# Kernel tuning notes

Measured on AMD Instinct MI355X. Metric: run time of the kernel, lower is better.

The kernel has to match this reference:

```python
import jax, jax.numpy as jnp
import numpy as np

B, S, H, D = 4, 2048, 16, 128

def setup_inputs() -> dict:
    key = jax.random.key(0)
    kq, kk, kv = jax.random.split(key, 3)
    shape = (B, S, H, D)
    return {
        "q": jax.random.normal(kq, shape, dtype=jnp.float32),
        "k": jax.random.normal(kk, shape, dtype=jnp.float32),
        "v": jax.random.normal(kv, shape, dtype=jnp.float32),
    }

def reference(q, k, v):
    # Fused recurrent linear attention (causal, unnormalized):
    #   H_t = H_{t-1} + k_t v_t^T ;  o_t = (scale * q_t) @ H_t
    scale = jnp.asarray(q.shape[-1], q.dtype) ** -0.5
    # move seq axis to front for scan: [S, B, H, D]
    qs = jnp.moveaxis(q, 1, 0) * scale
    ks = jnp.moveaxis(k, 1, 0)
    vs = jnp.moveaxis(v, 1, 0)

    def step(h, qkv):
        qt, kt, vt = qkv  # each [B, H, D]
        h = h + kt[..., :, None] * vt[..., None, :]  # [B, H, Dk, Dv]
        o = jnp.einsum('bhk,bhkv->bhv', qt, h)       # [B, H, Dv]
        return h, o

    h0 = jnp.zeros((q.shape[0], q.shape[2], q.shape[3], v.shape[3]), dtype=q.dtype)
    _, o = jax.lax.scan(step, h0, (qs, ks, vs))
    return jnp.moveaxis(o, 0, 1)  # [B, S, H, D]
```

## Files before the change

kernel.cpp:

```cpp
#include <hip/hip_runtime.h>


#define Bc 4
#define Sq 2048
#define Hh 16
#define Dd 128
#define RS (Hh * Dd)
#define Cc 128
#define NCH (Sq / Cc)
#define BHt (Bc * Hh)

using frag_ab = __attribute__((ext_vector_type(8))) short;
using frag_cd = __attribute__((ext_vector_type(4))) float;

__device__ __forceinline__ unsigned short f2bf(float f) {
  union { float f; unsigned u; } x; x.f = f;
  unsigned r = x.u + 0x7FFFu + ((x.u >> 16) & 1u);
  return (unsigned short)(r >> 16);
}
__device__ __forceinline__ float bf2f(unsigned short h) {
  union { unsigned u; float f; } x; x.u = ((unsigned)h) << 16; return x.f;
}
__device__ __forceinline__ int sw64(int r, int c) {
  return r * 64 + ((((c >> 3) ^ (r & 7)) << 3) | (c & 7));
}
__device__ __forceinline__ int sw128(int r, int c) {
  return r * 128 + ((((c >> 3) ^ (r & 15)) << 3) | (c & 7));
}

#define SCALE 0.08838834764831845f

__global__ __launch_bounds__(256) void ph1_ktv(const float* __restrict__ kg,
                                               const float* __restrict__ vg,
                                               unsigned short* __restrict__ st) {
  __shared__ unsigned short KT[128 * 64];
  __shared__ unsigned short VT[128 * 64];
  const int tid = threadIdx.x;
  const int bid = blockIdx.x;
  const int bh = bid >> 4, n = bid & 15;
  const int b = bh >> 4, h = bh & 15;
  const size_t cbase = (size_t)b * Sq * RS + (size_t)n * Cc * RS + (size_t)h * Dd;
  const int w = tid >> 6, L = tid & 63;
  const int wr = w >> 1, wc = w & 1, li = L & 15, q4 = L >> 4;

  frag_cd acc[4][4];
#pragma unroll
  for (int i = 0; i < 4; ++i)
#pragma unroll
    for (int j = 0; j < 4; ++j) acc[i][j] = (frag_cd){0.f, 0.f, 0.f, 0.f};

  for (int half = 0; half < 2; ++half) {
    __syncthreads();
#pragma unroll
    for (int it = 0; it < 8; ++it) {
      const int sl = (tid & 15) | ((it & 3) << 4);
      const int c0 = ((tid >> 4) | ((it >> 2) << 4)) << 2;
      const int t = 64 * half + sl;
      const float4 k4 = *(const float4*)(kg + cbase + (size_t)t * RS + c0);
      const float4 v4 = *(const float4*)(vg + cbase + (size_t)t * RS + c0);
      KT[sw64(c0 + 0, sl)] = f2bf(k4.x);
      KT[sw64(c0 + 1, sl)] = f2bf(k4.y);
      KT[sw64(c0 + 2, sl)] = f2bf(k4.z);
      KT[sw64(c0 + 3, sl)] = f2bf(k4.w);
      VT[sw64(c0 + 0, sl)] = f2bf(v4.x);
      VT[sw64(c0 + 1, sl)] = f2bf(v4.y);
      VT[sw64(c0 + 2, sl)] = f2bf(v4.z);
      VT[sw64(c0 + 3, sl)] = f2bf(v4.w);
    }
    __syncthreads();
#pragma unroll
    for (int kt = 0; kt < 2; ++kt) {
      frag_ab af[4], bf_[4];
#pragma unroll
      for (int mt = 0; mt < 4; ++mt)
        af[mt] = *(const frag_ab*)&VT[sw64(64 * wr + 16 * mt + li, 32 * kt + 8 * q4)];
#pragma unroll
      for (int nt = 0; nt < 4; ++nt)
        bf_[nt] = *(const frag_ab*)&KT[sw64(64 * wc + 16 * nt + li, 32 * kt + 8 * q4)];
#pragma unroll
      for (int mt = 0; mt < 4; ++mt)
#pragma unroll
        for (int nt = 0; nt < 4; ++nt)
          acc[mt][nt] = __builtin_amdgcn_mfma_f32_16x16x32_bf16(af[mt], bf_[nt], acc[mt][nt], 0, 0, 0);
    }
  }
  const size_t sb = (size_t)(bh * 16 + n) * (128 * 128);
#pragma unroll
  for (int mt = 0; mt < 4; ++mt)
#pragma unroll
    for (int nt = 0; nt < 4; ++nt)
#pragma unroll
      for (int r = 0; r < 4; ++r) {
        const int dv = 64 * wr + 16 * mt + 4 * q4 + r;
        const int dk = 64 * wc + 16 * nt + li;
        st[sb + (size_t)dv * 128 + dk] = f2bf(acc[mt][nt][r]);
      }
}

__global__ __launch_bounds__(256) void ph2_prefix(unsigned short* __restrict__ st) {
  const int bid = blockIdx.x;
  const int bh = bid >> 3, sl = bid & 7;
  const size_t base = (size_t)bh * NCH * (128 * 128) + (size_t)sl * 2048 +
                      (size_t)threadIdx.x * 8;
  float acc[8];
#pragma unroll
  for (int i = 0; i < 8; ++i) acc[i] = 0.f;
  for (int n = 0; n < NCH; ++n) {
    const size_t idx = base + (size_t)n * (128 * 128);
    const ushort4 s0 = *(const ushort4*)(st + idx);
    const ushort4 s1 = *(const ushort4*)(st + idx + 4);
    ushort4 h0, h1;
    h0.x = f2bf(acc[0]); h0.y = f2bf(acc[1]); h0.z = f2bf(acc[2]); h0.w = f2bf(acc[3]);
    h1.x = f2bf(acc[4]); h1.y = f2bf(acc[5]); h1.z = f2bf(acc[6]); h1.w = f2bf(acc[7]);
    *(ushort4*)(st + idx) = h0;
    *(ushort4*)(st + idx + 4) = h1;
    acc[0] += bf2f(s0.x); acc[1] += bf2f(s0.y); acc[2] += bf2f(s0.z); acc[3] += bf2f(s0.w);
    acc[4] += bf2f(s1.x); acc[5] += bf2f(s1.y); acc[6] += bf2f(s1.z); acc[7] += bf2f(s1.w);
  }
}

__global__ __launch_bounds__(256) void ph3a_intra(const float* __restrict__ qg,
                                                  const float* __restrict__ kg,
                                                  const float* __restrict__ vg,
                                                  float* __restrict__ o) {
  __shared__ unsigned short A_[128 * 64];
  __shared__ unsigned short B_[128 * 64];
  __shared__ unsigned short P_[128 * 128];
  const int tid = threadIdx.x;
  const int bid = blockIdx.x;
  const int bh = bid >> 4, n = bid & 15;
  const int b = bh >> 4, h = bh & 15;
  const size_t cbase = (size_t)b * Sq * RS + (size_t)n * Cc * RS + (size_t)h * Dd;
  const int w = tid >> 6, L = tid & 63;
  const int wr = w >> 1, wc = w & 1, li = L & 15, q4 = L >> 4;

  frag_cd acc[4][4];
#pragma unroll
  for (int i = 0; i < 4; ++i)
#pragma unroll
    for (int j = 0; j < 4; ++j) acc[i][j] = (frag_cd){0.f, 0.f, 0.f, 0.f};

  for (int half = 0; half < 2; ++half) {
    __syncthreads();
#pragma unroll
    for (int it = 0; it < 8; ++it) {
      const int f = it * 256 + tid;
      const int t = f >> 4;
      const int c0 = (f & 15) << 2;
      const float4 q4v = *(const float4*)(qg + cbase + (size_t)t * RS + 64 * half + c0);
      const float4 k4v = *(const float4*)(kg + cbase + (size_t)t * RS + 64 * half + c0);
      ushort4 qu, ku;
      qu.x = f2bf(q4v.x * SCALE); qu.y = f2bf(q4v.y * SCALE);
      qu.z = f2bf(q4v.z * SCALE); qu.w = f2bf(q4v.w * SCALE);
      ku.x = f2bf(k4v.x); ku.y = f2bf(k4v.y); ku.z = f2bf(k4v.z); ku.w = f2bf(k4v.w);
      *(ushort4*)&A_[sw64(t, c0)] = qu;
      *(ushort4*)&B_[sw64(t, c0)] = ku;
    }
    __syncthreads();
    if (64 * wc <= 64 * wr + 63) {
#pragma unroll
      for (int kt = 0; kt < 2; ++kt) {
        frag_ab af[4], bf_[4];
#pragma unroll
        for (int mt = 0; mt < 4; ++mt)
          af[mt] = *(const frag_ab*)&A_[sw64(64 * wr + 16 * mt + li, 32 * kt + 8 * q4)];
#pragma unroll
        for (int nt = 0; nt < 4; ++nt)
          bf_[nt] = *(const frag_ab*)&B_[sw64(64 * wc + 16 * nt + li, 32 * kt + 8 * q4)];
#pragma unroll
        for (int mt = 0; mt < 4; ++mt)
#pragma unroll
          for (int nt = 0; nt < 4; ++nt)
            if (64 * wc + 16 * nt <= 64 * wr + 16 * mt + 15)
              acc[mt][nt] = __builtin_amdgcn_mfma_f32_16x16x32_bf16(af[mt], bf_[nt], acc[mt][nt], 0, 0, 0);
      }
    }
  }
#pragma unroll
  for (int mt = 0; mt < 4; ++mt)
#pragma unroll
    for (int nt = 0; nt < 4; ++nt) {
      const int t0 = 64 * wr + 16 * mt + 4 * q4;
      const int s = 64 * wc + 16 * nt + li;
#pragma unroll
      for (int r = 0; r < 4; ++r) {
        const int t = t0 + r;
        P_[sw128(t, s)] = (s <= t) ? f2bf(acc[mt][nt][r]) : (unsigned short)0;
      }
    }
#pragma unroll
  for (int i = 0; i < 4; ++i)
#pragma unroll
    for (int j = 0; j < 4; ++j) acc[i][j] = (frag_cd){0.f, 0.f, 0.f, 0.f};

  for (int half = 0; half < 2; ++half) {
    __syncthreads();
#pragma unroll
    for (int it = 0; it < 8; ++it) {
      const int sl = (tid & 15) | ((it & 3) << 4);
      const int c0 = ((tid >> 4) | ((it >> 2) << 4)) << 2;
      const int s = 64 * half + sl;
      const float4 v4v = *(const float4*)(vg + cbase + (size_t)s * RS + c0);
      A_[sw64(c0 + 0, sl)] = f2bf(v4v.x);
      A_[sw64(c0 + 1, sl)] = f2bf(v4v.y);
      A_[sw64(c0 + 2, sl)] = f2bf(v4v.z);
      A_[sw64(c0 + 3, sl)] = f2bf(v4v.w);
    }
    __syncthreads();
#pragma unroll
    for (int kt = 0; kt < 2; ++kt) {
      const int ktg = 2 * half + kt;
      if (32 * ktg > 64 * wr + 63) continue;
      frag_ab af[4], bf_[4];
#pragma unroll
      for (int mt = 0; mt < 4; ++mt)
        af[mt] = *(const frag_ab*)&P_[sw128(64 * wr + 16 * mt + li, 32 * ktg + 8 * q4)];
#pragma unroll
      for (int nt = 0; nt < 4; ++nt)
        bf_[nt] = *(const frag_ab*)&A_[sw64(64 * wc + 16 * nt + li, 32 * kt + 8 * q4)];
#pragma unroll
      for (int mt = 0; mt < 4; ++mt)
#pragma unroll
        for (int nt = 0; nt < 4; ++nt)
          if (32 * ktg <= 64 * wr + 16 * mt + 15)
            acc[mt][nt] = __builtin_amdgcn_mfma_f32_16x16x32_bf16(af[mt], bf_[nt], acc[mt][nt], 0, 0, 0);
    }
  }
#pragma unroll
  for (int mt = 0; mt < 4; ++mt)
#pragma unroll
    for (int nt = 0; nt < 4; ++nt)
#pragma unroll
      for (int r = 0; r < 4; ++r) {
        const int t = 64 * wr + 16 * mt + 4 * q4 + r;
        const int dv = 64 * wc + 16 * nt + li;
        o[cbase + (size_t)t * RS + dv] = acc[mt][nt][r];
      }
}

__global__ __launch_bounds__(256) void ph3b_inter(const float* __restrict__ qg,
                                                  const unsigned short* __restrict__ st,
                                                  float* __restrict__ o) {
  __shared__ unsigned short Qf[128 * 128];
  __shared__ unsigned short Hb[128 * 64];
  const int tid = threadIdx.x;
  const int bid = blockIdx.x;
  const int bh = bid >> 4, n = bid & 15;
  const int b = bh >> 4, h = bh & 15;
  const size_t cbase = (size_t)b * Sq * RS + (size_t)n * Cc * RS + (size_t)h * Dd;
  const size_t sb = (size_t)(bh * 16 + n) * (128 * 128);
  const int w = tid >> 6, L = tid & 63;
  const int wr = w >> 1, wc = w & 1, li = L & 15, q4 = L >> 4;

#pragma unroll
  for (int it = 0; it < 16; ++it) {
    const int f = it * 256 + tid;
    const int t = f >> 5;
    const int c0 = (f & 31) << 2;
    const float4 q4v = *(const float4*)(qg + cbase + (size_t)t * RS + c0);
    ushort4 qu;
    qu.x = f2bf(q4v.x * SCALE); qu.y = f2bf(q4v.y * SCALE);
    qu.z = f2bf(q4v.z * SCALE); qu.w = f2bf(q4v.w * SCALE);
    *(ushort4*)&Qf[sw128(t, c0)] = qu;
  }
  frag_cd acc[4][4];
#pragma unroll
  for (int i = 0; i < 4; ++i)
#pragma unroll
    for (int j = 0; j < 4; ++j) acc[i][j] = (frag_cd){0.f, 0.f, 0.f, 0.f};

  for (int half = 0; half < 2; ++half) {
    __syncthreads();
#pragma unroll
    for (int it = 0; it < 4; ++it) {
      const int f = it * 256 + tid;
      const int dv = f >> 3;
      const int c8 = (f & 7) << 3;
      const uint4 hv = *(const uint4*)(st + sb + (size_t)dv * 128 + 64 * half + c8);
      *(uint4*)&Hb[sw64(dv, c8)] = hv;
    }
    __syncthreads();
#pragma unroll
    for (int kt = 0; kt < 2; ++kt) {
      const int ktg = 2 * half + kt;
      frag_ab af[4], bf_[4];
#pragma unroll
      for (int mt = 0; mt < 4; ++mt)
        af[mt] = *(const frag_ab*)&Qf[sw128(64 * wr + 16 * mt + li, 32 * ktg + 8 * q4)];
#pragma unroll
      for (int nt = 0; nt < 4; ++nt)
        bf_[nt] = *(const frag_ab*)&Hb[sw64(64 * wc + 16 * nt + li, 32 * kt + 8 * q4)];
#pragma unroll
      for (int mt = 0; mt < 4; ++mt)
#pragma unroll
        for (int nt = 0; nt < 4; ++nt)
          acc[mt][nt] = __builtin_amdgcn_mfma_f32_16x16x32_bf16(af[mt], bf_[nt], acc[mt][nt], 0, 0, 0);
    }
  }
#pragma unroll
  for (int mt = 0; mt < 4; ++mt)
#pragma unroll
    for (int nt = 0; nt < 4; ++nt)
#pragma unroll
      for (int r = 0; r < 4; ++r) {
        const int t = 64 * wr + 16 * mt + 4 * q4 + r;
        const int dv = 64 * wc + 16 * nt + li;
        const size_t oi = cbase + (size_t)t * RS + dv;
        o[oi] += acc[mt][nt][r];
      }
}

extern "C" void kernel_launch(void* const* d_in, const int* in_sizes, int n_in,
                              void* d_out, int out_size, void* d_ws, size_t ws_size,
                              hipStream_t stream) {
  const float* q = (const float*)d_in[0];
  const float* k = (const float*)d_in[1];
  const float* v = (const float*)d_in[2];
  float* o = (float*)d_out;
  unsigned short* st = (unsigned short*)d_ws;
  hipLaunchKernelGGL(ph1_ktv, dim3(BHt * NCH), dim3(256), 0, stream, k, v, st);
  hipLaunchKernelGGL(ph2_prefix, dim3(BHt * 8), dim3(256), 0, stream, st);
  hipLaunchKernelGGL(ph3a_intra, dim3(BHt * NCH), dim3(256), 0, stream, q, k, v, o);
  hipLaunchKernelGGL(ph3b_inter, dim3(BHt * NCH), dim3(256), 0, stream, q, st, o);
}
```

Before: 289.0 us.

## Fuse chunk-state and prefix scan into one kernel; merge intra and inter output kernels

Replaces the four-kernel chunked pipeline with two kernels. The first gives each block one 16-row dv slice of a head and walks all chunks in order, keeping the running state in MFMA accumulators with a register prefetch of the next chunk, so it writes prefix states directly and the separate prefix-scan pass and its extra state traffic disappear. The second computes the inter-chunk term q·H and the causal intra-chunk term in one kernel, reusing the bf16 Q tile and writing the output once rather than storing it and then doing a read-modify-write. In exchange the state kernel has only 512 blocks, each running a serial loop over 16 chunks, and the output kernel carries two accumulator sets, which raises register pressure.

```diff
diff --git a/kernel.cpp b/kernel.cpp
--- a/kernel.cpp
+++ b/kernel.cpp
@@ -9,6 +9,7 @@
 #define Cc 128
 #define NCH (Sq / Cc)
 #define BHt (Bc * Hh)
+#define SCALE 0.08838834764831845f
 
 using frag_ab = __attribute__((ext_vector_type(8))) short;
 using frag_cd = __attribute__((ext_vector_type(4))) float;
@@ -18,231 +19,109 @@
   unsigned r = x.u + 0x7FFFu + ((x.u >> 16) & 1u);
   return (unsigned short)(r >> 16);
 }
-__device__ __forceinline__ float bf2f(unsigned short h) {
-  union { unsigned u; float f; } x; x.u = ((unsigned)h) << 16; return x.f;
-}
 __device__ __forceinline__ int sw64(int r, int c) {
   return r * 64 + ((((c >> 3) ^ (r & 7)) << 3) | (c & 7));
 }
 __device__ __forceinline__ int sw128(int r, int c) {
   return r * 128 + ((((c >> 3) ^ (r & 15)) << 3) | (c & 7));
 }
-
-#define SCALE 0.08838834764831845f
-
-__global__ __launch_bounds__(256) void ph1_ktv(const float* __restrict__ kg,
+__device__ __forceinline__ int swKT(int dk, int t) {
+  return dk * 128 + ((((t >> 3) ^ (dk ^ (dk >> 4))) & 15) << 3) + (t & 7);
+}
+__device__ __forceinline__ int swVT(int dv, int t) {
+  return dv * 128 + ((((t >> 3) ^ dv) & 15) << 3) + (t & 7);
+}
+
+__global__ __launch_bounds__(256) void phA_state(const float* __restrict__ kg,
+                                                 const float* __restrict__ vg,
+                                                 unsigned short* __restrict__ st) {
+  __shared__ unsigned short KT[128 * 128];
+  __shared__ unsigned short VT[16 * 128];
+  const int tid = threadIdx.x;
+  const int bh = blockIdx.x & 63, slice = blockIdx.x >> 6;
+  const int b = bh >> 4, h = bh & 15;
+  const int dv0 = slice * 16;
+  const size_t base = (size_t)b * Sq * RS + (size_t)h * Dd;
+  const int w = tid >> 6, L = tid & 63, li = L & 15, q4 = L >> 4;
+  const int kdk0 = (tid & 31) * 4;
+  const int ktg4 = (tid >> 5) * 4;
+  const int vdv0l = (tid & 3) * 4;
+  const int vt0 = (tid >> 2) * 2;
+
+  float4 rk[4][4];
+  float4 rv[2];
+  auto prefetch = [&](int n) {
+    const size_t t0g = (size_t)n * Cc;
+#pragma unroll
+    for (int p = 0; p < 4; ++p) {
+      const int t0 = p * 32 + ktg4;
+#pragma unroll
+      for (int i = 0; i < 4; ++i)
+        rk[p][i] = *(const float4*)(kg + base + (t0g + t0 + i) * (size_t)RS + kdk0);
+    }
+#pragma unroll
+    for (int i = 0; i < 2; ++i)
+      rv[i] = *(const float4*)(vg + base + (t0g + vt0 + i) * (size_t)RS + dv0 + vdv0l);
+  };
+
+  frag_cd acc[2];
+  acc[0] = (frag_cd){0.f, 0.f, 0.f, 0.f};
+  acc[1] = (frag_cd){0.f, 0.f, 0.f, 0.f};
+  prefetch(0);
+  const size_t sbb = (size_t)bh * NCH * (128 * 128);
+
+  for (int n = 0; n < NCH; ++n) {
+    __syncthreads();
+#pragma unroll
+    for (int p = 0; p < 4; ++p) {
+      const int t0 = p * 32 + ktg4;
+#pragma unroll
+      for (int j = 0; j < 4; ++j) {
+        ushort4 u;
+        u.x = f2bf(((const float*)&rk[p][0])[j]);
+        u.y = f2bf(((const float*)&rk[p][1])[j]);
+        u.z = f2bf(((const float*)&rk[p][2])[j]);
+        u.w = f2bf(((const float*)&rk[p][3])[j]);
+        *(ushort4*)&KT[swKT(kdk0 + j, t0)] = u;
+      }
+    }
+#pragma unroll
+    for (int j = 0; j < 4; ++j) {
+      ushort2 u;
+      u.x = f2bf(((const float*)&rv[0])[j]);
+      u.y = f2bf(((const float*)&rv[1])[j]);
+      *(ushort2*)&VT[swVT(vdv0l + j, vt0)] = u;
+    }
+    if (n + 1 < NCH) prefetch(n + 1);
+    __syncthreads();
+    const size_t sb = sbb + (size_t)n * (128 * 128);
+#pragma unroll
+    for (int nt = 0; nt < 2; ++nt)
+#pragma unroll
+      for (int r = 0; r < 4; ++r) {
+        const int dv = dv0 + 4 * q4 + r;
+        const int dk = 32 * w + 16 * nt + li;
+        st[sb + (size_t)dv * 128 + dk] = f2bf(acc[nt][r]);
+      }
+#pragma unroll
+    for (int kt = 0; kt < 4; ++kt) {
+      frag_ab af = *(const frag_ab*)&VT[swVT(li, 32 * kt + 8 * q4)];
+#pragma unroll
+      for (int nt = 0; nt < 2; ++nt) {
+        frag_ab bf = *(const frag_ab*)&KT[swKT(32 * w + 16 * nt + li, 32 * kt + 8 * q4)];
+        acc[nt] = __builtin_amdgcn_mfma_f32_16x16x32_bf16(af, bf, acc[nt], 0, 0, 0);
+      }
+    }
+  }
+}
+
+__global__ __launch_bounds__(256) void phB_out(const float* __restrict__ qg,
+                                               const float* __restrict__ kg,
                                                const float* __restrict__ vg,
-                                               unsigned short* __restrict__ st) {
-  __shared__ unsigned short KT[128 * 64];
-  __shared__ unsigned short VT[128 * 64];
-  const int tid = threadIdx.x;
-  const int bid = blockIdx.x;
-  const int bh = bid >> 4, n = bid & 15;
-  const int b = bh >> 4, h = bh & 15;
-  const size_t cbase = (size_t)b * Sq * RS + (size_t)n * Cc * RS + (size_t)h * Dd;
-  const int w = tid >> 6, L = tid & 63;
-  const int wr = w >> 1, wc = w & 1, li = L & 15, q4 = L >> 4;
-
-  frag_cd acc[4][4];
-#pragma unroll
-  for (int i = 0; i < 4; ++i)
-#pragma unroll
-    for (int j = 0; j < 4; ++j) acc[i][j] = (frag_cd){0.f, 0.f, 0.f, 0.f};
-
-  for (int half = 0; half < 2; ++half) {
-    __syncthreads();
-#pragma unroll
-    for (int it = 0; it < 8; ++it) {
-      const int sl = (tid & 15) | ((it & 3) << 4);
-      const int c0 = ((tid >> 4) | ((it >> 2) << 4)) << 2;
-      const int t = 64 * half + sl;
-      const float4 k4 = *(const float4*)(kg + cbase + (size_t)t * RS + c0);
-      const float4 v4 = *(const float4*)(vg + cbase + (size_t)t * RS + c0);
-      KT[sw64(c0 + 0, sl)] = f2bf(k4.x);
-      KT[sw64(c0 + 1, sl)] = f2bf(k4.y);
-      KT[sw64(c0 + 2, sl)] = f2bf(k4.z);
-      KT[sw64(c0 + 3, sl)] = f2bf(k4.w);
-      VT[sw64(c0 + 0, sl)] = f2bf(v4.x);
-      VT[sw64(c0 + 1, sl)] = f2bf(v4.y);
-      VT[sw64(c0 + 2, sl)] = f2bf(v4.z);
-      VT[sw64(c0 + 3, sl)] = f2bf(v4.w);
-    }
-    __syncthreads();
-#pragma unroll
-    for (int kt = 0; kt < 2; ++kt) {
-      frag_ab af[4], bf_[4];
-#pragma unroll
-      for (int mt = 0; mt < 4; ++mt)
-        af[mt] = *(const frag_ab*)&VT[sw64(64 * wr + 16 * mt + li, 32 * kt + 8 * q4)];
-#pragma unroll
-      for (int nt = 0; nt < 4; ++nt)
-        bf_[nt] = *(const frag_ab*)&KT[sw64(64 * wc + 16 * nt + li, 32 * kt + 8 * q4)];
-#pragma unroll
-      for (int mt = 0; mt < 4; ++mt)
-#pragma unroll
-        for (int nt = 0; nt < 4; ++nt)
-          acc[mt][nt] = __builtin_amdgcn_mfma_f32_16x16x32_bf16(af[mt], bf_[nt], acc[mt][nt], 0, 0, 0);
-    }
-  }
-  const size_t sb = (size_t)(bh * 16 + n) * (128 * 128);
-#pragma unroll
-  for (int mt = 0; mt < 4; ++mt)
-#pragma unroll
-    for (int nt = 0; nt < 4; ++nt)
-#pragma unroll
-      for (int r = 0; r < 4; ++r) {
-        const int dv = 64 * wr + 16 * mt + 4 * q4 + r;
-        const int dk = 64 * wc + 16 * nt + li;
-        st[sb + (size_t)dv * 128 + dk] = f2bf(acc[mt][nt][r]);
-      }
-}
-
-__global__ __launch_bounds__(256) void ph2_prefix(unsigned short* __restrict__ st) {
-  const int bid = blockIdx.x;
-  const int bh = bid >> 3, sl = bid & 7;
-  const size_t base = (size_t)bh * NCH * (128 * 128) + (size_t)sl * 2048 +
-                      (size_t)threadIdx.x * 8;
-  float acc[8];
-#pragma unroll
-  for (int i = 0; i < 8; ++i) acc[i] = 0.f;
-  for (int n = 0; n < NCH; ++n) {
-    const size_t idx = base + (size_t)n * (128 * 128);
-    const ushort4 s0 = *(const ushort4*)(st + idx);
-    const ushort4 s1 = *(const ushort4*)(st + idx + 4);
-    ushort4 h0, h1;
-    h0.x = f2bf(acc[0]); h0.y = f2bf(acc[1]); h0.z = f2bf(acc[2]); h0.w = f2bf(acc[3]);
-    h1.x = f2bf(acc[4]); h1.y = f2bf(acc[5]); h1.z = f2bf(acc[6]); h1.w = f2bf(acc[7]);
-    *(ushort4*)(st + idx) = h0;
-    *(ushort4*)(st + idx + 4) = h1;
-    acc[0] += bf2f(s0.x); acc[1] += bf2f(s0.y); acc[2] += bf2f(s0.z); acc[3] += bf2f(s0.w);
-    acc[4] += bf2f(s1.x); acc[5] += bf2f(s1.y); acc[6] += bf2f(s1.z); acc[7] += bf2f(s1.w);
-  }
-}
-
-__global__ __launch_bounds__(256) void ph3a_intra(const float* __restrict__ qg,
-                                                  const float* __restrict__ kg,
-                                                  const float* __restrict__ vg,
-                                                  float* __restrict__ o) {
-  __shared__ unsigned short A_[128 * 64];
-  __shared__ unsigned short B_[128 * 64];
-  __shared__ unsigned short P_[128 * 128];
-  const int tid = threadIdx.x;
-  const int bid = blockIdx.x;
-  const int bh = bid >> 4, n = bid & 15;
-  const int b = bh >> 4, h = bh & 15;
-  const size_t cbase = (size_t)b * Sq * RS + (size_t)n * Cc * RS + (size_t)h * Dd;
-  const int w = tid >> 6, L = tid & 63;
-  const int wr = w >> 1, wc = w & 1, li = L & 15, q4 = L >> 4;
-
-  frag_cd acc[4][4];
-#pragma unroll
-  for (int i = 0; i < 4; ++i)
-#pragma unroll
-    for (int j = 0; j < 4; ++j) acc[i][j] = (frag_cd){0.f, 0.f, 0.f, 0.f};
-
-  for (int half = 0; half < 2; ++half) {
-    __syncthreads();
-#pragma unroll
-    for (int it = 0; it < 8; ++it) {
-      const int f = it * 256 + tid;
-      const int t = f >> 4;
-      const int c0 = (f & 15) << 2;
-      const float4 q4v = *(const float4*)(qg + cbase + (size_t)t * RS + 64 * half + c0);
-      const float4 k4v = *(const float4*)(kg + cbase + (size_t)t * RS + 64 * half + c0);
-      ushort4 qu, ku;
-      qu.x = f2bf(q4v.x * SCALE); qu.y = f2bf(q4v.y * SCALE);
-      qu.z = f2bf(q4v.z * SCALE); qu.w = f2bf(q4v.w * SCALE);
-      ku.x = f2bf(k4v.x); ku.y = f2bf(k4v.y); ku.z = f2bf(k4v.z); ku.w = f2bf(k4v.w);
-      *(ushort4*)&A_[sw64(t, c0)] = qu;
-      *(ushort4*)&B_[sw64(t, c0)] = ku;
-    }
-    __syncthreads();
-    if (64 * wc <= 64 * wr + 63) {
-#pragma unroll
-      for (int kt = 0; kt < 2; ++kt) {
-        frag_ab af[4], bf_[4];
-#pragma unroll
-        for (int mt = 0; mt < 4; ++mt)
-          af[mt] = *(const frag_ab*)&A_[sw64(64 * wr + 16 * mt + li, 32 * kt + 8 * q4)];
-#pragma unroll
-        for (int nt = 0; nt < 4; ++nt)
-          bf_[nt] = *(const frag_ab*)&B_[sw64(64 * wc + 16 * nt + li, 32 * kt + 8 * q4)];
-#pragma unroll
-        for (int mt = 0; mt < 4; ++mt)
-#pragma unroll
-          for (int nt = 0; nt < 4; ++nt)
-            if (64 * wc + 16 * nt <= 64 * wr + 16 * mt + 15)
-              acc[mt][nt] = __builtin_amdgcn_mfma_f32_16x16x32_bf16(af[mt], bf_[nt], acc[mt][nt], 0, 0, 0);
-      }
-    }
-  }
-#pragma unroll
-  for (int mt = 0; mt < 4; ++mt)
-#pragma unroll
-    for (int nt = 0; nt < 4; ++nt) {
-      const int t0 = 64 * wr + 16 * mt + 4 * q4;
-      const int s = 64 * wc + 16 * nt + li;
-#pragma unroll
-      for (int r = 0; r < 4; ++r) {
-        const int t = t0 + r;
-        P_[sw128(t, s)] = (s <= t) ? f2bf(acc[mt][nt][r]) : (unsigned short)0;
-      }
-    }
-#pragma unroll
-  for (int i = 0; i < 4; ++i)
-#pragma unroll
-    for (int j = 0; j < 4; ++j) acc[i][j] = (frag_cd){0.f, 0.f, 0.f, 0.f};
-
-  for (int half = 0; half < 2; ++half) {
-    __syncthreads();
-#pragma unroll
-    for (int it = 0; it < 8; ++it) {
-      const int sl = (tid & 15) | ((it & 3) << 4);
-      const int c0 = ((tid >> 4) | ((it >> 2) << 4)) << 2;
-      const int s = 64 * half + sl;
-      const float4 v4v = *(const float4*)(vg + cbase + (size_t)s * RS + c0);
-      A_[sw64(c0 + 0, sl)] = f2bf(v4v.x);
-      A_[sw64(c0 + 1, sl)] = f2bf(v4v.y);
-      A_[sw64(c0 + 2, sl)] = f2bf(v4v.z);
-      A_[sw64(c0 + 3, sl)] = f2bf(v4v.w);
-    }
-    __syncthreads();
-#pragma unroll
-    for (int kt = 0; kt < 2; ++kt) {
-      const int ktg = 2 * half + kt;
-      if (32 * ktg > 64 * wr + 63) continue;
-      frag_ab af[4], bf_[4];
-#pragma unroll
-      for (int mt = 0; mt < 4; ++mt)
-        af[mt] = *(const frag_ab*)&P_[sw128(64 * wr + 16 * mt + li, 32 * ktg + 8 * q4)];
-#pragma unroll
-      for (int nt = 0; nt < 4; ++nt)
-        bf_[nt] = *(const frag_ab*)&A_[sw64(64 * wc + 16 * nt + li, 32 * kt + 8 * q4)];
-#pragma unroll
-      for (int mt = 0; mt < 4; ++mt)
-#pragma unroll
-        for (int nt = 0; nt < 4; ++nt)
-          if (32 * ktg <= 64 * wr + 16 * mt + 15)
-            acc[mt][nt] = __builtin_amdgcn_mfma_f32_16x16x32_bf16(af[mt], bf_[nt], acc[mt][nt], 0, 0, 0);
-    }
-  }
-#pragma unroll
-  for (int mt = 0; mt < 4; ++mt)
-#pragma unroll
-    for (int nt = 0; nt < 4; ++nt)
-#pragma unroll
-      for (int r = 0; r < 4; ++r) {
-        const int t = 64 * wr + 16 * mt + 4 * q4 + r;
-        const int dv = 64 * wc + 16 * nt + li;
-        o[cbase + (size_t)t * RS + dv] = acc[mt][nt][r];
-      }
-}
-
-__global__ __launch_bounds__(256) void ph3b_inter(const float* __restrict__ qg,
-                                                  const unsigned short* __restrict__ st,
-                                                  float* __restrict__ o) {
-  __shared__ unsigned short Qf[128 * 128];
-  __shared__ unsigned short Hb[128 * 64];
+                                               const unsigned short* __restrict__ st,
+                                               float* __restrict__ o) {
+  __shared__ unsigned short QP[128 * 128];
+  __shared__ unsigned short Bb[128 * 64];
   const int tid = threadIdx.x;
   const int bid = blockIdx.x;
   const int bh = bid >> 4, n = bid & 15;
@@ -261,13 +140,16 @@
     ushort4 qu;
     qu.x = f2bf(q4v.x * SCALE); qu.y = f2bf(q4v.y * SCALE);
     qu.z = f2bf(q4v.z * SCALE); qu.w = f2bf(q4v.w * SCALE);
-    *(ushort4*)&Qf[sw128(t, c0)] = qu;
-  }
-  frag_cd acc[4][4];
+    *(ushort4*)&QP[sw128(t, c0)] = qu;
+  }
+  frag_cd accO[4][4], accP[4][4];
 #pragma unroll
   for (int i = 0; i < 4; ++i)
 #pragma unroll
-    for (int j = 0; j < 4; ++j) acc[i][j] = (frag_cd){0.f, 0.f, 0.f, 0.f};
+    for (int j = 0; j < 4; ++j) {
+      accO[i][j] = (frag_cd){0.f, 0.f, 0.f, 0.f};
+      accP[i][j] = (frag_cd){0.f, 0.f, 0.f, 0.f};
+    }
 
   for (int half = 0; half < 2; ++half) {
     __syncthreads();
@@ -277,7 +159,7 @@
       const int dv = f >> 3;
       const int c8 = (f & 7) << 3;
       const uint4 hv = *(const uint4*)(st + sb + (size_t)dv * 128 + 64 * half + c8);
-      *(uint4*)&Hb[sw64(dv, c8)] = hv;
+      *(uint4*)&Bb[sw64(dv, c8)] = hv;
     }
     __syncthreads();
 #pragma unroll
@@ -286,15 +168,96 @@
       frag_ab af[4], bf_[4];
 #pragma unroll
       for (int mt = 0; mt < 4; ++mt)
-        af[mt] = *(const frag_ab*)&Qf[sw128(64 * wr + 16 * mt + li, 32 * ktg + 8 * q4)];
+        af[mt] = *(const frag_ab*)&QP[sw128(64 * wr + 16 * mt + li, 32 * ktg + 8 * q4)];
 #pragma unroll
       for (int nt = 0; nt < 4; ++nt)
-        bf_[nt] = *(const frag_ab*)&Hb[sw64(64 * wc + 16 * nt + li, 32 * kt + 8 * q4)];
+        bf_[nt] = *(const frag_ab*)&Bb[sw64(64 * wc + 16 * nt + li, 32 * kt + 8 * q4)];
 #pragma unroll
       for (int mt = 0; mt < 4; ++mt)
 #pragma unroll
         for (int nt = 0; nt < 4; ++nt)
-          acc[mt][nt] = __builtin_amdgcn_mfma_f32_16x16x32_bf16(af[mt], bf_[nt], acc[mt][nt], 0, 0, 0);
+          accO[mt][nt] = __builtin_amdgcn_mfma_f32_16x16x32_bf16(af[mt], bf_[nt], accO[mt][nt], 0, 0, 0);
+    }
+  }
+
+  for (int half = 0; half < 2; ++half) {
+    __syncthreads();
+#pragma unroll
+    for (int it = 0; it < 8; ++it) {
+      const int f = it * 256 + tid;
+      const int t = f >> 4;
+      const int c0 = (f & 15) << 2;
+      const float4 k4v = *(const float4*)(kg + cbase + (size_t)t * RS + 64 * half + c0);
+      ushort4 ku;
+      ku.x = f2bf(k4v.x); ku.y = f2bf(k4v.y); ku.z = f2bf(k4v.z); ku.w = f2bf(k4v.w);
+      *(ushort4*)&Bb[sw64(t, c0)] = ku;
+    }
+    __syncthreads();
+    if (64 * wc <= 64 * wr + 63) {
+#pragma unroll
+      for (int kt = 0; kt < 2; ++kt) {
+        const int ktg = 2 * half + kt;
+        frag_ab af[4], bf_[4];
+#pragma unroll
+        for (int mt = 0; mt < 4; ++mt)
+          af[mt] = *(const frag_ab*)&QP[sw128(64 * wr + 16 * mt + li, 32 * ktg + 8 * q4)];
+#pragma unroll
+        for (int nt = 0; nt < 4; ++nt)
+          bf_[nt] = *(const frag_ab*)&Bb[sw64(64 * wc + 16 * nt + li, 32 * kt + 8 * q4)];
+#pragma unroll
+        for (int mt = 0; mt < 4; ++mt)
+#pragma unroll
+          for (int nt = 0; nt < 4; ++nt)
+            if (64 * wc + 16 * nt <= 64 * wr + 16 * mt + 15)
+              accP[mt][nt] = __builtin_amdgcn_mfma_f32_16x16x32_bf16(af[mt], bf_[nt], accP[mt][nt], 0, 0, 0);
+      }
+    }
+  }
+  __syncthreads();
+#pragma unroll
+  for (int mt = 0; mt < 4; ++mt)
+#pragma unroll
+    for (int nt = 0; nt < 4; ++nt) {
+      const int t0 = 64 * wr + 16 * mt + 4 * q4;
+      const int s = 64 * wc + 16 * nt + li;
+#pragma unroll
+      for (int r = 0; r < 4; ++r) {
+        const int t = t0 + r;
+        QP[sw128(t, s)] = (s <= t) ? f2bf(accP[mt][nt][r]) : (unsigned short)0;
+      }
+    }
+
+  for (int half = 0; half < 2; ++half) {
+    __syncthreads();
+#pragma unroll
+    for (int it = 0; it < 8; ++it) {
+      const int sl = (tid & 15) | ((it & 3) << 4);
+      const int c0 = ((tid >> 4) | ((it >> 2) << 4)) << 2;
+      const int s = 64 * half + sl;
+      const float4 v4v = *(const float4*)(vg + cbase + (size_t)s * RS + c0);
+      Bb[sw64(c0 + 0, sl)] = f2bf(v4v.x);
+      Bb[sw64(c0 + 1, sl)] = f2bf(v4v.y);
+      Bb[sw64(c0 + 2, sl)] = f2bf(v4v.z);
+      Bb[sw64(c0 + 3, sl)] = f2bf(v4v.w);
+    }
+    __syncthreads();
+#pragma unroll
+    for (int kt = 0; kt < 2; ++kt) {
+      const int ktg = 2 * half + kt;
+      if (32 * ktg > 64 * wr + 63) continue;
+      frag_ab af[4], bf_[4];
+#pragma unroll
+      for (int mt = 0; mt < 4; ++mt)
+        af[mt] = *(const frag_ab*)&QP[sw128(64 * wr + 16 * mt + li, 32 * ktg + 8 * q4)];
+#pragma unroll
+      for (int nt = 0; nt < 4; ++nt)
+        bf_[nt] = *(const frag_ab*)&Bb[sw64(64 * wc + 16 * nt + li, 32 * kt + 8 * q4)];
+#pragma unroll
+      for (int mt = 0; mt < 4; ++mt)
+#pragma unroll
+        for (int nt = 0; nt < 4; ++nt)
+          if (32 * ktg <= 64 * wr + 16 * mt + 15)
+            accO[mt][nt] = __builtin_amdgcn_mfma_f32_16x16x32_bf16(af[mt], bf_[nt], accO[mt][nt], 0, 0, 0);
     }
   }
 #pragma unroll
@@ -305,8 +268,7 @@
       for (int r = 0; r < 4; ++r) {
         const int t = 64 * wr + 16 * mt + 4 * q4 + r;
         const int dv = 64 * wc + 16 * nt + li;
-        const size_t oi = cbase + (size_t)t * RS + dv;
-        o[oi] += acc[mt][nt][r];
+        o[cbase + (size_t)t * RS + dv] = accO[mt][nt][r];
       }
 }
 
@@ -318,8 +280,6 @@
   const float* v = (const float*)d_in[2];
   float* o = (float*)d_out;
   unsigned short* st = (unsigned short*)d_ws;
-  hipLaunchKernelGGL(ph1_ktv, dim3(BHt * NCH), dim3(256), 0, stream, k, v, st);
-  hipLaunchKernelGGL(ph2_prefix, dim3(BHt * 8), dim3(256), 0, stream, st);
-  hipLaunchKernelGGL(ph3a_intra, dim3(BHt * NCH), dim3(256), 0, stream, q, k, v, o);
-  hipLaunchKernelGGL(ph3b_inter, dim3(BHt * NCH), dim3(256), 0, stream, q, st, o);
-}
+  hipLaunchKernelGGL(phA_state, dim3(BHt * 8), dim3(256), 0, stream, k, v, st);
+  hipLaunchKernelGGL(phB_out, dim3(BHt * NCH), dim3(256), 0, stream, q, k, v, st, o);
+}
```

New measurement: 274.9 us. -4.9%, faster.
